# Optimization experiments

Hardware: AMD Instinct MI355X
Metric: run time of the kernel (lower is better)

## Reference

```python
import jax, jax.numpy as jnp
import numpy as np

N_NODES = 10000
N_EDGES = 160000
N_TYPES = 128          # rows in SymbolicEmbeddingsVQ table
N_SYMBOLS = 64
PATTERN_LEN = 8
SYMBOL_DIM = 16
HIDDEN = PATTERN_LEN * SYMBOL_DIM  # mode='concat' -> 128
NUM_RADIAL = 6


def setup_inputs() -> dict:
    key = jax.random.key(0)
    ks = jax.random.split(key, 10)
    x = jax.random.randint(ks[0], (N_NODES,), 0, N_TYPES)
    rbf = jax.random.normal(ks[1], (N_EDGES, NUM_RADIAL), dtype=jnp.float32)
    i = jax.random.randint(ks[2], (N_EDGES,), 0, N_NODES)
    j = jax.random.randint(ks[3], (N_EDGES,), 0, N_NODES)
    # VQ symbolic embedding params: each of 128 types is a pattern of
    # PATTERN_LEN symbol ids; symbols are vectors from a codebook.
    code_idx = jax.random.randint(ks[4], (N_TYPES, PATTERN_LEN), 0, N_SYMBOLS)
    codebook = jax.random.normal(ks[5], (N_SYMBOLS, SYMBOL_DIM), dtype=jnp.float32)
    # Linear layers (PyTorch Linear default uniform init approximated by scaled normals)
    W_rbf = jax.random.normal(ks[6], (NUM_RADIAL, HIDDEN), dtype=jnp.float32) / np.sqrt(NUM_RADIAL)
    b_rbf = jnp.zeros((HIDDEN,), dtype=jnp.float32)
    W = jax.random.normal(ks[7], (3 * HIDDEN, HIDDEN), dtype=jnp.float32) / np.sqrt(3 * HIDDEN)
    b = jnp.zeros((HIDDEN,), dtype=jnp.float32)
    return {"x": x, "rbf": rbf, "i": i, "j": j, "code_idx": code_idx,
            "codebook": codebook, "W_rbf": W_rbf, "b_rbf": b_rbf, "W": W, "b": b}


def reference(x, rbf, i, j, code_idx, codebook, W_rbf, b_rbf, W, b):
    act = jax.nn.silu
    # Symbolic VQ embedding, mode='concat': table[t] = concat of PATTERN_LEN codebook vectors
    table = codebook[code_idx].reshape(N_TYPES, HIDDEN)   # [128, hidden]
    h = table[x]                                          # [N_nodes, hidden]
    r = act(rbf @ W_rbf + b_rbf)                          # [E, hidden]
    feat = jnp.concatenate([h[i], h[j], r], axis=-1)      # [E, 3*hidden]
    return act(feat @ W + b)                              # [E, hidden]
```

## Files before the change

### kernel.cpp

```cpp
#include <hip/hip_runtime.h>
#include <hip/hip_bf16.h>
#include <stdint.h>

typedef __attribute__((ext_vector_type(8))) short bf16x8;
typedef __attribute__((ext_vector_type(4))) float f32x4;
typedef __attribute__((ext_vector_type(4))) unsigned short u16x4;

__device__ __forceinline__ float silu_f(float x) {
    return x * __builtin_amdgcn_rcpf(1.0f + __expf(-x));
}

__device__ __forceinline__ unsigned short f2bf(float x) {
    union { float f; unsigned int u; } v; v.f = x;
    unsigned int r = v.u + 0x7fffu + ((v.u >> 16) & 1u);
    return (unsigned short)(r >> 16);
}
__device__ __forceinline__ float bf2f(unsigned short u) {
    union { unsigned int u; float f; } v; v.u = ((unsigned int)u) << 16;
    return v.f;
}

__device__ __forceinline__ void async16(void* l, const void* g) {
    auto lds3 = (__attribute__((address_space(3))) unsigned int*)(uintptr_t)l;
    auto g1   = (const __attribute__((address_space(1))) unsigned int*)(uintptr_t)g;
    __builtin_amdgcn_global_load_lds(g1, lds3, 16, 0, 0);
}

__global__ void prep_P(const int* __restrict__ code_idx,
                       const float* __restrict__ codebook,
                       const float* __restrict__ W,
                       const float* __restrict__ b,
                       unsigned short* __restrict__ P1,
                       unsigned short* __restrict__ P2,
                       unsigned short* __restrict__ Wt3)
{
    __shared__ float trow[128];
    const int t = blockIdx.x, tid = threadIdx.x;
    if (tid < 128) {
        int sym = code_idx[t * 8 + (tid >> 4)];
        trow[tid] = codebook[sym * 16 + (tid & 15)];
    } else {
        int k = tid - 128;
        Wt3[t * 128 + k] = f2bf(W[(256 + k) * 128 + t]);
    }
    __syncthreads();
    const int which = tid >> 7, o = tid & 127;
    const float* Wb = W + which * 16384;
    float acc = which ? 0.0f : b[o];
#pragma unroll 8
    for (int k = 0; k < 128; ++k)
        acc += trow[k] * Wb[k * 128 + o];
    (which ? P2 : P1)[t * 128 + o] = f2bf(acc);
}

__global__ __launch_bounds__(256, 3) void fused_main(
    const int* __restrict__ x,
    const float* __restrict__ rbf,
    const int* __restrict__ ei,
    const int* __restrict__ ej,
    const float* __restrict__ W_rbf,
    const float* __restrict__ b_rbf,
    const unsigned short* __restrict__ P1,
    const unsigned short* __restrict__ P2,
    const unsigned short* __restrict__ Wt3,
    float* __restrict__ out)
{
    __shared__ __align__(16) unsigned char lB[32768];
    __shared__ __align__(16) unsigned char lA[16384];
    __shared__ __align__(16) unsigned char lR[1536];

    const int tid  = threadIdx.x;
    const int lane = tid & 63;
    const int w    = tid >> 6;
    const int e0   = blockIdx.x * 64;

    const int quad = lane >> 4, l15 = lane & 15;
    const int wm = (w >> 1) * 32, wn = (w & 1) * 64;

    {
        const int ri = lane >> 4, ch = lane & 15;
#pragma unroll
        for (int rr = 0; rr < 8; ++rr) {
            int g = w * 8 + rr;
            int o = g * 4 + ri;
            int j = ch ^ (o & 7);
            async16(lB + g * 1024, Wt3 + o * 128 + j * 8);
        }
    }
    if (w == 0)
        async16(lR, (const unsigned char*)rbf + (size_t)e0 * 24 + lane * 16);
    else if (w == 1 && lane < 32)
        async16(lR + 1024, (const unsigned char*)rbf + (size_t)e0 * 24 + 1024 + lane * 16);

    int ti[2], tj[2];
#pragma unroll
    for (int mi = 0; mi < 2; ++mi) {
        int e = e0 + wm + mi * 16 + l15;
        ti[mi] = x[ei[e]];
        tj[mi] = x[ej[e]];
    }

    const int j16 = tid & 15, gg = tid >> 4, cb = j16 * 8;
    float wr[6][8], br[8];
#pragma unroll
    for (int q = 0; q < 6; ++q) {
        const float4* p = (const float4*)(W_rbf + q * 128 + cb);
        float4 a = p[0], c = p[1];
        wr[q][0]=a.x; wr[q][1]=a.y; wr[q][2]=a.z; wr[q][3]=a.w;
        wr[q][4]=c.x; wr[q][5]=c.y; wr[q][6]=c.z; wr[q][7]=c.w;
    }
    {
        const float4* p = (const float4*)(b_rbf + cb);
        float4 a = p[0], c = p[1];
        br[0]=a.x; br[1]=a.y; br[2]=a.z; br[3]=a.w;
        br[4]=c.x; br[5]=c.y; br[6]=c.z; br[7]=c.w;
    }

    __syncthreads();

#pragma unroll
    for (int i = 0; i < 4; ++i) {
        int m = gg * 4 + i;
        const float* rr_ = (const float*)(lR + m * 24);
        float f0 = rr_[0], f1 = rr_[1], f2 = rr_[2],
              f3 = rr_[3], f4 = rr_[4], f5 = rr_[5];
        bf16x8 pk;
#pragma unroll
        for (int c = 0; c < 8; ++c) {
            float a = br[c] + f0*wr[0][c] + f1*wr[1][c] + f2*wr[2][c]
                            + f3*wr[3][c] + f4*wr[4][c] + f5*wr[5][c];
            pk[c] = (short)f2bf(silu_f(a));
        }
        int p = j16 ^ (m & 7);
        *(bf16x8*)(lA + m * 256 + p * 16) = pk;
    }

    __syncthreads();

    u16x4 q1[2][4], q2[2][4];
#pragma unroll
    for (int mi = 0; mi < 2; ++mi) {
        const unsigned short* p1r = P1 + ti[mi] * 128;
        const unsigned short* p2r = P2 + tj[mi] * 128;
#pragma unroll
        for (int ni = 0; ni < 4; ++ni) {
            int o = wn + ni * 16 + quad * 4;
            q1[mi][ni] = *(const u16x4*)(p1r + o);
            q2[mi][ni] = *(const u16x4*)(p2r + o);
        }
    }

    f32x4 acc[2][4] = {};
    const int l7 = l15 & 7;
#pragma unroll
    for (int ks = 0; ks < 4; ++ks) {
        const int j = ks * 4 + quad;
        const int p = j ^ l7;
        bf16x8 af[2], bfv[4];
#pragma unroll
        for (int mi = 0; mi < 2; ++mi)
            af[mi] = *(const bf16x8*)(lA + (wm + mi * 16 + l15) * 256 + p * 16);
#pragma unroll
        for (int ni = 0; ni < 4; ++ni)
            bfv[ni] = *(const bf16x8*)(lB + (wn + ni * 16 + l15) * 256 + p * 16);
#pragma unroll
        for (int mi = 0; mi < 2; ++mi)
#pragma unroll
            for (int ni = 0; ni < 4; ++ni)
                acc[mi][ni] = __builtin_amdgcn_mfma_f32_16x16x32_bf16(
                    bfv[ni], af[mi], acc[mi][ni], 0, 0, 0);
    }

#pragma unroll
    for (int mi = 0; mi < 2; ++mi) {
        size_t e = (size_t)(e0 + wm + mi * 16 + l15);
        float* orow = out + e * 128 + wn;
#pragma unroll
        for (int ni = 0; ni < 4; ++ni) {
            f32x4 v;
#pragma unroll
            for (int r = 0; r < 4; ++r)
                v[r] = silu_f(acc[mi][ni][r]
                              + bf2f(q1[mi][ni][r]) + bf2f(q2[mi][ni][r]));
            *(f32x4*)(orow + ni * 16 + quad * 4) = v;
        }
    }
}

extern "C" void kernel_launch(void* const* d_in, const int* in_sizes, int n_in,
                              void* d_out, int out_size, void* d_ws, size_t ws_size,
                              hipStream_t stream) {
    const int*   x        = (const int*)d_in[0];
    const float* rbf      = (const float*)d_in[1];
    const int*   ei       = (const int*)d_in[2];
    const int*   ej       = (const int*)d_in[3];
    const int*   code_idx = (const int*)d_in[4];
    const float* codebook = (const float*)d_in[5];
    const float* W_rbf    = (const float*)d_in[6];
    const float* b_rbf    = (const float*)d_in[7];
    const float* W        = (const float*)d_in[8];
    const float* b        = (const float*)d_in[9];
    float* out = (float*)d_out;

    const int nE = in_sizes[2];

    if (ws_size < 98304) return;
    unsigned short* P1  = (unsigned short*)d_ws;
    unsigned short* P2  = P1 + 16384;
    unsigned short* Wt3 = P2 + 16384;

    prep_P<<<128, 256, 0, stream>>>(code_idx, codebook, W, b, P1, P2, Wt3);
    fused_main<<<nE / 64, 256, 0, stream>>>(x, rbf, ei, ej, W_rbf, b_rbf,
                                            P1, P2, Wt3, out);
}
```

Before: 142.9 us.

## Process four edge tiles per block with double-buffered rbf and index prefetch

```diff
diff --git a/kernel.cpp b/kernel.cpp
--- a/kernel.cpp
+++ b/kernel.cpp
@@ -67,12 +67,12 @@
 {
     __shared__ __align__(16) unsigned char lB[32768];
     __shared__ __align__(16) unsigned char lA[16384];
-    __shared__ __align__(16) unsigned char lR[1536];
+    __shared__ __align__(16) unsigned char lR[2][1536];
 
     const int tid  = threadIdx.x;
     const int lane = tid & 63;
     const int w    = tid >> 6;
-    const int e0   = blockIdx.x * 64;
+    const int base = blockIdx.x * 256;
 
     const int quad = lane >> 4, l15 = lane & 15;
     const int wm = (w >> 1) * 32, wn = (w & 1) * 64;
@@ -83,19 +83,20 @@
         for (int rr = 0; rr < 8; ++rr) {
             int g = w * 8 + rr;
             int o = g * 4 + ri;
-            int j = ch ^ (o & 7);
-            async16(lB + g * 1024, Wt3 + o * 128 + j * 8);
+            int jc = ch ^ (o & 7);
+            async16(lB + g * 1024, Wt3 + o * 128 + jc * 8);
         }
     }
     if (w == 0)
-        async16(lR, (const unsigned char*)rbf + (size_t)e0 * 24 + lane * 16);
+        async16(lR[0], (const unsigned char*)rbf + (size_t)base * 24 + lane * 16);
     else if (w == 1 && lane < 32)
-        async16(lR + 1024, (const unsigned char*)rbf + (size_t)e0 * 24 + 1024 + lane * 16);
+        async16(lR[0] + 1024,
+                (const unsigned char*)rbf + (size_t)base * 24 + 1024 + lane * 16);
 
     int ti[2], tj[2];
 #pragma unroll
     for (int mi = 0; mi < 2; ++mi) {
-        int e = e0 + wm + mi * 16 + l15;
+        int e = base + wm + mi * 16 + l15;
         ti[mi] = x[ei[e]];
         tj[mi] = x[ej[e]];
     }
@@ -119,70 +120,98 @@
     __syncthreads();
 
 #pragma unroll
-    for (int i = 0; i < 4; ++i) {
-        int m = gg * 4 + i;
-        const float* rr_ = (const float*)(lR + m * 24);
-        float f0 = rr_[0], f1 = rr_[1], f2 = rr_[2],
-              f3 = rr_[3], f4 = rr_[4], f5 = rr_[5];
-        bf16x8 pk;
-#pragma unroll
-        for (int c = 0; c < 8; ++c) {
-            float a = br[c] + f0*wr[0][c] + f1*wr[1][c] + f2*wr[2][c]
-                            + f3*wr[3][c] + f4*wr[4][c] + f5*wr[5][c];
-            pk[c] = (short)f2bf(silu_f(a));
-        }
-        int p = j16 ^ (m & 7);
-        *(bf16x8*)(lA + m * 256 + p * 16) = pk;
-    }
-
-    __syncthreads();
-
-    u16x4 q1[2][4], q2[2][4];
-#pragma unroll
-    for (int mi = 0; mi < 2; ++mi) {
-        const unsigned short* p1r = P1 + ti[mi] * 128;
-        const unsigned short* p2r = P2 + tj[mi] * 128;
-#pragma unroll
-        for (int ni = 0; ni < 4; ++ni) {
-            int o = wn + ni * 16 + quad * 4;
-            q1[mi][ni] = *(const u16x4*)(p1r + o);
-            q2[mi][ni] = *(const u16x4*)(p2r + o);
-        }
-    }
-
-    f32x4 acc[2][4] = {};
-    const int l7 = l15 & 7;
-#pragma unroll
-    for (int ks = 0; ks < 4; ++ks) {
-        const int j = ks * 4 + quad;
-        const int p = j ^ l7;
-        bf16x8 af[2], bfv[4];
-#pragma unroll
-        for (int mi = 0; mi < 2; ++mi)
-            af[mi] = *(const bf16x8*)(lA + (wm + mi * 16 + l15) * 256 + p * 16);
-#pragma unroll
-        for (int ni = 0; ni < 4; ++ni)
-            bfv[ni] = *(const bf16x8*)(lB + (wn + ni * 16 + l15) * 256 + p * 16);
-#pragma unroll
-        for (int mi = 0; mi < 2; ++mi)
+    for (int t = 0; t < 4; ++t) {
+        const int e0 = base + t * 64;
+
+        int nti[2], ntj[2];
+        if (t < 3) {
+            const unsigned char* src =
+                (const unsigned char*)rbf + (size_t)(e0 + 64) * 24;
+            if (w == 0)
+                async16(lR[(t + 1) & 1], src + lane * 16);
+            else if (w == 1 && lane < 32)
+                async16(lR[(t + 1) & 1] + 1024, src + 1024 + lane * 16);
+#pragma unroll
+            for (int mi = 0; mi < 2; ++mi) {
+                int e = e0 + 64 + wm + mi * 16 + l15;
+                nti[mi] = x[ei[e]];
+                ntj[mi] = x[ej[e]];
+            }
+        }
+
+#pragma unroll
+        for (int i = 0; i < 4; ++i) {
+            int m = gg * 4 + i;
+            const float* rr_ = (const float*)(lR[t & 1] + m * 24);
+            float f0 = rr_[0], f1 = rr_[1], f2 = rr_[2],
+                  f3 = rr_[3], f4 = rr_[4], f5 = rr_[5];
+            bf16x8 pk;
+#pragma unroll
+            for (int c = 0; c < 8; ++c) {
+                float a = br[c] + f0*wr[0][c] + f1*wr[1][c] + f2*wr[2][c]
+                                + f3*wr[3][c] + f4*wr[4][c] + f5*wr[5][c];
+                pk[c] = (short)f2bf(silu_f(a));
+            }
+            int p = j16 ^ (m & 7);
+            *(bf16x8*)(lA + m * 256 + p * 16) = pk;
+        }
+
+        __syncthreads();
+
+        u16x4 q1[2][4], q2[2][4];
+#pragma unroll
+        for (int mi = 0; mi < 2; ++mi) {
+            const unsigned short* p1r = P1 + ti[mi] * 128;
+            const unsigned short* p2r = P2 + tj[mi] * 128;
+#pragma unroll
+            for (int ni = 0; ni < 4; ++ni) {
+                int o = wn + ni * 16 + quad * 4;
+                q1[mi][ni] = *(const u16x4*)(p1r + o);
+                q2[mi][ni] = *(const u16x4*)(p2r + o);
+            }
+        }
+
+        f32x4 acc[2][4] = {};
+        const int l7 = l15 & 7;
+#pragma unroll
+        for (int ks = 0; ks < 4; ++ks) {
+            const int j = ks * 4 + quad;
+            const int p = j ^ l7;
+            bf16x8 af[2], bfv[4];
+#pragma unroll
+            for (int mi = 0; mi < 2; ++mi)
+                af[mi] = *(const bf16x8*)(lA + (wm + mi * 16 + l15) * 256 + p * 16);
 #pragma unroll
             for (int ni = 0; ni < 4; ++ni)
-                acc[mi][ni] = __builtin_amdgcn_mfma_f32_16x16x32_bf16(
-                    bfv[ni], af[mi], acc[mi][ni], 0, 0, 0);
-    }
-
-#pragma unroll
-    for (int mi = 0; mi < 2; ++mi) {
-        size_t e = (size_t)(e0 + wm + mi * 16 + l15);
-        float* orow = out + e * 128 + wn;
-#pragma unroll
-        for (int ni = 0; ni < 4; ++ni) {
-            f32x4 v;
-#pragma unroll
-            for (int r = 0; r < 4; ++r)
-                v[r] = silu_f(acc[mi][ni][r]
-                              + bf2f(q1[mi][ni][r]) + bf2f(q2[mi][ni][r]));
-            *(f32x4*)(orow + ni * 16 + quad * 4) = v;
+                bfv[ni] = *(const bf16x8*)(lB + (wn + ni * 16 + l15) * 256 + p * 16);
+#pragma unroll
+            for (int mi = 0; mi < 2; ++mi)
+#pragma unroll
+                for (int ni = 0; ni < 4; ++ni)
+                    acc[mi][ni] = __builtin_amdgcn_mfma_f32_16x16x32_bf16(
+                        bfv[ni], af[mi], acc[mi][ni], 0, 0, 0);
+        }
+
+        __syncthreads();
+
+#pragma unroll
+        for (int mi = 0; mi < 2; ++mi) {
+            size_t e = (size_t)(e0 + wm + mi * 16 + l15);
+            float* orow = out + e * 128 + wn;
+#pragma unroll
+            for (int ni = 0; ni < 4; ++ni) {
+                f32x4 v;
+#pragma unroll
+                for (int r = 0; r < 4; ++r)
+                    v[r] = silu_f(acc[mi][ni][r]
+                                  + bf2f(q1[mi][ni][r]) + bf2f(q2[mi][ni][r]));
+                *(f32x4*)(orow + ni * 16 + quad * 4) = v;
+            }
+        }
+
+        if (t < 3) {
+#pragma unroll
+            for (int mi = 0; mi < 2; ++mi) { ti[mi] = nti[mi]; tj[mi] = ntj[mi]; }
         }
     }
 }
@@ -210,6 +239,6 @@
     unsigned short* Wt3 = P2 + 16384;
 
     prep_P<<<128, 256, 0, stream>>>(code_idx, codebook, W, b, P1, P2, Wt3);
-    fused_main<<<nE / 64, 256, 0, stream>>>(x, rbf, ei, ej, W_rbf, b_rbf,
-                                            P1, P2, Wt3, out);
-}
+    fused_main<<<nE / 256, 256, 0, stream>>>(x, rbf, ei, ej, W_rbf, b_rbf,
+                                             P1, P2, Wt3, out);
+}
```

After: 153.0 us. 1.07x slower.
